# Kernel optimization log

Hardware: AMD Instinct MI355X
Metric: run time of the kernel (lower is better)

Reference implementation:

```python
import jax, jax.numpy as jnp
import numpy as np

D_MODEL = 768
NUM_HEADS = 12
HEAD_DIM = D_MODEL // NUM_HEADS
ROPE_THETA = 10000.0
MAX_SEQ_LEN = 2048
BATCH = 2
SEQ = 2048


def _rope_tables():
    # powers = arange(0, d_k, 2)/d_k ; freqs = theta**-powers ; angles = t outer freqs
    powers = jnp.arange(0, HEAD_DIM, 2, dtype=jnp.float32) / HEAD_DIM
    freqs = 1.0 / (ROPE_THETA ** powers)                      # [d_k/2]
    t = jnp.arange(MAX_SEQ_LEN, dtype=jnp.float32)
    angles = t[:, None] * freqs[None, :]                      # [max_seq_len, d_k/2]
    return jnp.cos(angles), jnp.sin(angles)


def _apply_rope(x, cos, sin, pos):
    # x: [b, h, s, d], pos: [b, s]; interleaved even/odd pairing
    c = cos[pos][:, None]          # [b, 1, s, d/2]
    s = sin[pos][:, None]
    x_even = x[..., 0::2]
    x_odd = x[..., 1::2]
    new_even = x_even * c - x_odd * s
    new_odd = x_even * s + x_odd * c
    # re-interleave: (..., f, 2) -> (..., 2f)
    return jnp.stack([new_even, new_odd], axis=-1).reshape(x.shape)


def setup_inputs() -> dict:
    key = jax.random.key(0)
    k1, k2, k3 = jax.random.split(key, 3)
    x = jax.random.normal(k1, (BATCH, SEQ, D_MODEL), dtype=jnp.float32)
    token_positions = jnp.broadcast_to(jnp.arange(SEQ, dtype=jnp.int32), (BATCH, SEQ))
    sigma_qkv = (2.0 / (D_MODEL + 3 * D_MODEL)) ** 0.5
    sigma_o = (2.0 / (D_MODEL + D_MODEL)) ** 0.5
    W_qkv = jax.random.normal(k2, (3 * D_MODEL, D_MODEL), dtype=jnp.float32) * sigma_qkv
    W_o = jax.random.normal(k3, (D_MODEL, D_MODEL), dtype=jnp.float32) * sigma_o
    return {"x": x, "token_positions": token_positions, "W_qkv": W_qkv, "W_o": W_o}


def reference(x, token_positions, W_qkv, W_o):
    b, s, _ = x.shape
    cos, sin = _rope_tables()
    qkv = jnp.einsum('bsd,ed->bse', x, W_qkv)                 # [b, s, 3*d_model]
    qkv = qkv.reshape(b, s, 3, NUM_HEADS, HEAD_DIM)
    qkv = jnp.transpose(qkv, (2, 0, 3, 1, 4))                 # [3, b, h, s, hd]
    q, k, v = qkv[0], qkv[1], qkv[2]
    q = _apply_rope(q, cos, sin, token_positions)
    k = _apply_rope(k, cos, sin, token_positions)
    scores = jnp.einsum('bhqd,bhkd->bhqk', q, k) / (HEAD_DIM ** 0.5)
    causal = jnp.tril(jnp.ones((s, s), dtype=bool))
    scores = jnp.where(causal, scores, -jnp.inf)
    weights = jax.nn.softmax(scores, axis=-1)
    context = jnp.einsum('bhqk,bhkd->bhqd', weights, v)
    context = jnp.transpose(context, (0, 2, 1, 3)).reshape(b, s, D_MODEL)
    return jnp.einsum('bsd,ed->bse', context, W_o)
```

## Files before the change

### kernel.cpp

```cpp
#include <hip/hip_runtime.h>
#include <hip/hip_bf16.h>
#include <math.h>

#define SEQ 2048
#define DM 768
#define NH 12
#define HD 64
#define NB 2
#define NT (NB*SEQ)
#define E3 (3*DM)

using short4v = __attribute__((ext_vector_type(4))) short;
using short8v = __attribute__((ext_vector_type(8))) short;
using floatx4 = __attribute__((ext_vector_type(4))) float;
using int4v   = __attribute__((ext_vector_type(4))) int;

#if __has_builtin(__builtin_amdgcn_exp2f)
#define EXPFN(x) __builtin_amdgcn_exp2f(x)
#define QSCALE 0.1803368801111244f
#else
#define EXPFN(x) __expf(x)
#define QSCALE 0.125f
#endif

static __device__ __forceinline__ short bfb(float f) {
  union { __hip_bfloat16 h; short s; } u;
  u.h = __float2bfloat16(f);
  return u.s;
}

static __device__ __forceinline__ void gload_lds16(const __hip_bfloat16* g, __hip_bfloat16* lds) {
  __builtin_amdgcn_global_load_lds(
      (const __attribute__((address_space(1))) unsigned int*)g,
      (__attribute__((address_space(3))) unsigned int*)lds, 16, 0, 0);
}

static __device__ __forceinline__ int swzg(int row) {
  return (((row >> 3) & 3) + 2 * (row & 3)) & 7;
}

#define XN4 (NT * DM / 4)
#define WQN4 (E3 * DM / 4)
#define WON4 (DM * DM / 4)
#define CVT_N (XN4 + WQN4 + WON4)
__global__ void cvt3_rope(const float* __restrict__ x, const float* __restrict__ wq,
                          const float* __restrict__ wo,
                          __hip_bfloat16* __restrict__ xb, __hip_bfloat16* __restrict__ wqb,
                          __hip_bfloat16* __restrict__ wob, float2* __restrict__ rcs,
                          int* __restrict__ qcnt) {
  int i = blockIdx.x * blockDim.x + threadIdx.x;
  if (blockIdx.x == 0 && threadIdx.x < 8) qcnt[threadIdx.x] = 0;
  if (i >= CVT_N) {
    int idx = i - CVT_N;
    if (idx < SEQ * 32) {
      int pos = idx >> 5, j = idx & 31;
      float freq = __expf(-(float)j * (logf(10000.0f) / 32.0f));
      float ang = (float)pos * freq;
      rcs[idx] = make_float2(cosf(ang), sinf(ang));
    }
    return;
  }
  const float* src;
  __hip_bfloat16* dst;
  int k;
  if (i < XN4) { src = x; dst = xb; k = i; }
  else if (i < XN4 + WQN4) { src = wq; dst = wqb; k = i - XN4; }
  else { src = wo; dst = wob; k = i - XN4 - WQN4; }
  floatx4 v = ((const floatx4*)src)[k];
  short4v o;
  o[0] = bfb(v[0]); o[1] = bfb(v[1]); o[2] = bfb(v[2]); o[3] = bfb(v[3]);
  ((short4v*)dst)[k] = o;
}

__global__ __launch_bounds__(256) void qkv_gemm_rope(
    const __hip_bfloat16* __restrict__ Wq,
    const __hip_bfloat16* __restrict__ Xb,
    const int* __restrict__ tpos,
    const float2* __restrict__ rcs,
    __hip_bfloat16* __restrict__ Qb, __hip_bfloat16* __restrict__ Kb,
    __hip_bfloat16* __restrict__ Vt)
{
  __shared__ __align__(16) __hip_bfloat16 As[2][64 * 64];
  __shared__ __align__(16) __hip_bfloat16 Bs[2][128 * 64];
  const int tid = threadIdx.x;
  const int lane = tid & 63, w = tid >> 6;
  const int c = lane & 15, g = lane >> 4;
  const int wr = w >> 1, wc = w & 1;
  const int bid = blockIdx.x;
  const int xcd = bid & 7, i_ = bid >> 3;
  const int nb = xcd * 4 + (i_ & 3), mb = i_ >> 2;
  const int m0 = mb * 64, n0 = nb * 128;
  const int srow = tid >> 3, sslot = tid & 7;

#define QKV_STAGE(K0_, AD, BD)                                                      \
  do {                                                                              \
    _Pragma("unroll")                                                               \
    for (int j = 0; j < 2; ++j) {                                                   \
      const int row = j * 32 + srow;                                                \
      const int gs = (sslot ^ (row & 7)) * 8;                                       \
      gload_lds16(Wq + (size_t)(m0 + row) * DM + (K0_) + gs, (AD) + j * 2048 + w * 512); \
    }                                                                               \
    _Pragma("unroll")                                                               \
    for (int j = 0; j < 4; ++j) {                                                   \
      const int row = j * 32 + srow;                                                \
      const int gs = (sslot ^ (row & 7)) * 8;                                       \
      gload_lds16(Xb + (size_t)(n0 + row) * DM + (K0_) + gs, (BD) + j * 2048 + w * 512); \
    }                                                                               \
  } while (0)

  floatx4 acc[2][4] = {};
  QKV_STAGE(0, As[0], Bs[0]);
  int cb = 0;
  for (int k0 = 0; k0 < DM; k0 += 64) {
    if (k0 + 64 < DM) QKV_STAGE(k0 + 64, As[cb ^ 1], Bs[cb ^ 1]);
    __syncthreads();
#pragma unroll
    for (int kk = 0; kk < 2; ++kk) {
      short8v a[2], b[4];
#pragma unroll
      for (int i = 0; i < 2; ++i) {
        const int row = wr * 32 + i * 16 + c;
        a[i] = *(const short8v*)&As[cb][row * 64 + (((kk * 4 + g) ^ (row & 7)) * 8)];
      }
#pragma unroll
      for (int j = 0; j < 4; ++j) {
        const int row = wc * 64 + j * 16 + c;
        b[j] = *(const short8v*)&Bs[cb][row * 64 + (((kk * 4 + g) ^ (row & 7)) * 8)];
      }
#pragma unroll
      for (int i = 0; i < 2; ++i)
#pragma unroll
        for (int j = 0; j < 4; ++j)
          acc[i][j] = __builtin_amdgcn_mfma_f32_16x16x32_bf16(a[i], b[j], acc[i][j], 0, 0, 0);
    }
    __syncthreads();
    cb ^= 1;
  }
#undef QKV_STAGE
#pragma unroll
  for (int i = 0; i < 2; ++i) {
    const int e0 = m0 + wr * 32 + i * 16 + 4 * g;
    const int jj = (e0 & 63) >> 1;
#pragma unroll
    for (int j = 0; j < 4; ++j) {
      const int t = n0 + wc * 64 + j * 16 + c;
      const int b_ = t >> 11, s = t & (SEQ - 1);
      float v0 = acc[i][j][0], v1 = acc[i][j][1], v2 = acc[i][j][2], v3 = acc[i][j][3];
      if (e0 < 2 * DM) {
        const int pos = tpos[t];
        const float2 cs0 = rcs[pos * 32 + jj];
        const float2 cs1 = rcs[pos * 32 + jj + 1];
        const float n0v = v0 * cs0.x - v1 * cs0.y, n1v = v0 * cs0.y + v1 * cs0.x;
        const float n2v = v2 * cs1.x - v3 * cs1.y, n3v = v2 * cs1.y + v3 * cs1.x;
        v0 = n0v; v1 = n1v; v2 = n2v; v3 = n3v;
      }
      if (e0 < DM) {
        const int h = e0 >> 6, d = e0 & 63;
        short4v pk;
        pk[0] = bfb(v0 * QSCALE); pk[1] = bfb(v1 * QSCALE);
        pk[2] = bfb(v2 * QSCALE); pk[3] = bfb(v3 * QSCALE);
        *(short4v*)&Qb[(((size_t)(b_ * NH + h) * SEQ) + s) * HD + d] = pk;
      } else if (e0 < 2 * DM) {
        const int e = e0 - DM, h = e >> 6, d = e & 63;
        short4v pk;
        pk[0] = bfb(v0); pk[1] = bfb(v1); pk[2] = bfb(v2); pk[3] = bfb(v3);
        *(short4v*)&Kb[(((size_t)(b_ * NH + h) * SEQ) + s) * HD + d] = pk;
      } else {
        const int e = e0 - 2 * DM, h = e >> 6, d = e & 63;
        const size_t base = ((size_t)(b_ * NH + h) * HD + d) * SEQ + s;
        Vt[base]           = __float2bfloat16(v0);
        Vt[base + SEQ]     = __float2bfloat16(v1);
        Vt[base + 2 * SEQ] = __float2bfloat16(v2);
        Vt[base + 3 * SEQ] = __float2bfloat16(v3);
      }
    }
  }
}

__global__ __launch_bounds__(512) void attn_fused(
    const __hip_bfloat16* __restrict__ Qb,
    const __hip_bfloat16* __restrict__ Kb,
    const __hip_bfloat16* __restrict__ Vt,
    __hip_bfloat16* __restrict__ Cx,
    int* __restrict__ qcnt)
{
  __shared__ __align__(16) __hip_bfloat16 Ks[2][128 * 64];
  __shared__ __align__(16) __hip_bfloat16 Vs[2][64 * 128];
  __shared__ int task_s;
  const int tid = threadIdx.x;
  const int lane = tid & 63, w = tid >> 6;
  const int c = lane & 15, g = lane >> 4;
  const int xcd = blockIdx.x & 7;
  const int kr1 = 8 * (c >> 2) + (c & 3);
  const int ksr = w * 8 + (lane >> 3), kss = lane & 7;
  const int vsr = w * 4 + (lane >> 4), vss = lane & 15;

  for (;;) {
    if (tid == 0) task_s = atomicAdd(&qcnt[xcd], 1);
    __syncthreads();
    const int task = task_s;
    if (task >= 48) return;
    const int qG = 15 - task / 3;
    const int bh = xcd + 8 * (task % 3);
    const int KBmax = qG;
    const __hip_bfloat16* Qh = Qb + (size_t)bh * SEQ * HD;
    const __hip_bfloat16* Kh = Kb + (size_t)bh * SEQ * HD;
    const __hip_bfloat16* Vh = Vt + (size_t)bh * HD * SEQ;
    const int q1 = qG * 128 + w * 16 + c;
    const int qrl32 = (w & 1) * 16 + c;
    const int sdiag = w >> 1;
    const short8v qf10 = *(const short8v*)&Qh[(size_t)q1 * HD + g * 8];
    const short8v qf11 = *(const short8v*)&Qh[(size_t)q1 * HD + 32 + g * 8];
    floatx4 o1[4] = {};
    float l1 = 0.0f;

#define STAGE_KV(KB_, KSD, VSD)                                                      \
    do {                                                                             \
      _Pragma("unroll")                                                              \
      for (int j = 0; j < 2; ++j) {                                                  \
        const int kr = j * 64 + ksr;                                                 \
        gload_lds16(Kh + (size_t)((KB_) * 128 + kr) * HD + ((kss ^ swzg(kr)) * 8),   \
                    (KSD) + j * 4096 + w * 512);                                     \
        const int vr = j * 32 + vsr;                                                 \
        gload_lds16(Vh + (size_t)vr * SEQ + (KB_) * 128 + ((vss ^ (vr & 15)) * 8),   \
                    (VSD) + j * 4096 + w * 512);                                     \
      }                                                                              \
    } while (0)

#define SUBBLK(S_, DO_MASK)                                                          \
    do {                                                                             \
      const int r0 = (S_) * 32 + kr1, r1 = r0 + 4;                                   \
      const int z0 = swzg(r0), z1 = swzg(r1);                                        \
      const short8v a00 = *(const short8v*)&Kt[r0 * 64 + ((g ^ z0) * 8)];            \
      const short8v a01 = *(const short8v*)&Kt[r0 * 64 + (((4 + g) ^ z0) * 8)];      \
      const short8v a10 = *(const short8v*)&Kt[r1 * 64 + ((g ^ z1) * 8)];            \
      const short8v a11 = *(const short8v*)&Kt[r1 * 64 + (((4 + g) ^ z1) * 8)];      \
      short8v vf[4];                                                                 \
      _Pragma("unroll")                                                              \
      for (int f = 0; f < 4; ++f) {                                                  \
        const int rv = f * 16 + c;                                                   \
        vf[f] = *(const short8v*)&Vb[rv * 128 + ((((S_) * 4 + g) ^ (rv & 15)) * 8)]; \
      }                                                                              \
      floatx4 s1a = {}, s1b = {};                                                    \
      __builtin_amdgcn_s_setprio(1);                                                 \
      s1a = __builtin_amdgcn_mfma_f32_16x16x32_bf16(a00, qf10, s1a, 0, 0, 0);        \
      s1a = __builtin_amdgcn_mfma_f32_16x16x32_bf16(a01, qf11, s1a, 0, 0, 0);        \
      s1b = __builtin_amdgcn_mfma_f32_16x16x32_bf16(a10, qf10, s1b, 0, 0, 0);        \
      s1b = __builtin_amdgcn_mfma_f32_16x16x32_bf16(a11, qf11, s1b, 0, 0, 0);        \
      __builtin_amdgcn_s_setprio(0);                                                 \
      if (DO_MASK) {                                                                 \
        _Pragma("unroll")                                                            \
        for (int r = 0; r < 4; ++r) {                                                \
          if (8 * g + r > qrl32) s1a[r] = -INFINITY;                                 \
          if (8 * g + r + 4 > qrl32) s1b[r] = -INFINITY;                             \
        }                                                                            \
      }                                                                              \
      short8v pf1;                                                                   \
      _Pragma("unroll")                                                              \
      for (int r = 0; r < 4; ++r) {                                                  \
        float p;                                                                     \
        p = EXPFN(s1a[r]); l1 += p; pf1[r] = bfb(p);                                 \
        p = EXPFN(s1b[r]); l1 += p; pf1[r + 4] = bfb(p);                             \
      }                                                                              \
      __builtin_amdgcn_s_setprio(1);                                                 \
      o1[0] = __builtin_amdgcn_mfma_f32_16x16x32_bf16(vf[0], pf1, o1[0], 0, 0, 0);   \
      o1[1] = __builtin_amdgcn_mfma_f32_16x16x32_bf16(vf[1], pf1, o1[1], 0, 0, 0);   \
      o1[2] = __builtin_amdgcn_mfma_f32_16x16x32_bf16(vf[2], pf1, o1[2], 0, 0, 0);   \
      o1[3] = __builtin_amdgcn_mfma_f32_16x16x32_bf16(vf[3], pf1, o1[3], 0, 0, 0);   \
      __builtin_amdgcn_s_setprio(0);                                                 \
    } while (0)

    STAGE_KV(0, Ks[0], Vs[0]);
    __syncthreads();
    int cb = 0;
    for (int kb = 0; kb <= KBmax; ++kb) {
      if (kb < KBmax) STAGE_KV(kb + 1, Ks[cb ^ 1], Vs[cb ^ 1]);
      {
        const __hip_bfloat16* Kt = Ks[cb];
        const __hip_bfloat16* Vb = Vs[cb];
        if (kb < KBmax) {
          SUBBLK(0, false);
          SUBBLK(1, false);
          SUBBLK(2, false);
          SUBBLK(3, false);
        } else {
#pragma unroll
          for (int s = 0; s < 4; ++s) {
            if (s < sdiag) SUBBLK(s, false);
            else if (s == sdiag) SUBBLK(s, true);
          }
        }
      }
      __syncthreads();
      cb ^= 1;
    }
#undef SUBBLK
#undef STAGE_KV

    l1 += __shfl_xor(l1, 16); l1 += __shfl_xor(l1, 32);
    const float inv1 = 1.0f / l1;
    const int bb = bh / NH, h = bh - bb * NH;
    const size_t trow1 = ((size_t)bb * SEQ + q1) * DM + (size_t)h * HD;
#pragma unroll
    for (int f = 0; f < 4; ++f) {
      short4v pk1;
#pragma unroll
      for (int r = 0; r < 4; ++r) pk1[r] = bfb(o1[f][r] * inv1);
      *(short4v*)&Cx[trow1 + f * 16 + 4 * g] = pk1;
    }
  }
}

__global__ __launch_bounds__(256) void out_gemm(
    const __hip_bfloat16* __restrict__ Wo,
    const __hip_bfloat16* __restrict__ Cx,
    float* __restrict__ out)
{
  __shared__ __align__(16) __hip_bfloat16 As[2][64 * 64];
  __shared__ __align__(16) __hip_bfloat16 Bs[2][128 * 64];
  const int tid = threadIdx.x;
  const int lane = tid & 63, w = tid >> 6;
  const int c = lane & 15, g = lane >> 4;
  const int wr = w >> 1, wc = w & 1;
  const int bid = blockIdx.x;
  const int xcd = bid & 7, i_ = bid >> 3;
  const int nb = xcd * 4 + (i_ & 3), mb = i_ >> 2;
  const int m0 = mb * 64, n0 = nb * 128;
  const int srow = tid >> 3, sslot = tid & 7;

#define OUT_STAGE(K0_, AD, BD)                                                      \
  do {                                                                              \
    _Pragma("unroll")                                                               \
    for (int j = 0; j < 2; ++j) {                                                   \
      const int row = j * 32 + srow;                                                \
      const int gs = (sslot ^ (row & 7)) * 8;                                       \
      gload_lds16(Wo + (size_t)(m0 + row) * DM + (K0_) + gs, (AD) + j * 2048 + w * 512); \
    }                                                                               \
    _Pragma("unroll")                                                               \
    for (int j = 0; j < 4; ++j) {                                                   \
      const int row = j * 32 + srow;                                                \
      const int gs = (sslot ^ (row & 7)) * 8;                                       \
      gload_lds16(Cx + (size_t)(n0 + row) * DM + (K0_) + gs, (BD) + j * 2048 + w * 512); \
    }                                                                               \
  } while (0)

  floatx4 acc[2][4] = {};
  OUT_STAGE(0, As[0], Bs[0]);
  int cb = 0;
  for (int k0 = 0; k0 < DM; k0 += 64) {
    if (k0 + 64 < DM) OUT_STAGE(k0 + 64, As[cb ^ 1], Bs[cb ^ 1]);
    __syncthreads();
#pragma unroll
    for (int kk = 0; kk < 2; ++kk) {
      short8v a[2], b[4];
#pragma unroll
      for (int i = 0; i < 2; ++i) {
        const int row = wr * 32 + i * 16 + c;
        a[i] = *(const short8v*)&As[cb][row * 64 + (((kk * 4 + g) ^ (row & 7)) * 8)];
      }
#pragma unroll
      for (int j = 0; j < 4; ++j) {
        const int row = wc * 64 + j * 16 + c;
        b[j] = *(const short8v*)&Bs[cb][row * 64 + (((kk * 4 + g) ^ (row & 7)) * 8)];
      }
#pragma unroll
      for (int i = 0; i < 2; ++i)
#pragma unroll
        for (int j = 0; j < 4; ++j)
          acc[i][j] = __builtin_amdgcn_mfma_f32_16x16x32_bf16(a[i], b[j], acc[i][j], 0, 0, 0);
    }
    __syncthreads();
    cb ^= 1;
  }
#undef OUT_STAGE
#pragma unroll
  for (int i = 0; i < 2; ++i) {
    const int e0 = m0 + wr * 32 + i * 16 + 4 * g;
#pragma unroll
    for (int j = 0; j < 4; ++j) {
      const int t = n0 + wc * 64 + j * 16 + c;
      *(floatx4*)&out[(size_t)t * DM + e0] = acc[i][j];
    }
  }
}

extern "C" void kernel_launch(void* const* d_in, const int* in_sizes, int n_in,
                              void* d_out, int out_size, void* d_ws, size_t ws_size,
                              hipStream_t stream) {
  const float* x    = (const float*)d_in[0];
  const int*   tpos = (const int*)d_in[1];
  const float* Wq   = (const float*)d_in[2];
  const float* Wo   = (const float*)d_in[3];
  float* out = (float*)d_out;

  const size_t QKV_BYTES = (size_t)NB * NH * SEQ * HD * 2;
  const size_t REQUIRED = 4 * QKV_BYTES;
  if (ws_size < REQUIRED) return;

  char* ws = (char*)d_ws;
  __hip_bfloat16* Qb = (__hip_bfloat16*)(ws);
  __hip_bfloat16* Kb = (__hip_bfloat16*)(ws + QKV_BYTES);
  __hip_bfloat16* Vt = (__hip_bfloat16*)(ws + 2 * QKV_BYTES);
  __hip_bfloat16* Cx = (__hip_bfloat16*)(ws + 3 * QKV_BYTES);
  __hip_bfloat16* xb = (__hip_bfloat16*)(ws + 3 * QKV_BYTES);
  char* ob = (char*)d_out;
  float2* rcs = (float2*)(ob);
  __hip_bfloat16* wqb = (__hip_bfloat16*)(ob + (size_t)SEQ * 32 * 8);
  __hip_bfloat16* wob = (__hip_bfloat16*)(ob + (size_t)SEQ * 32 * 8 + (size_t)E3 * DM * 2);
  int* qcnt = (int*)(ob + (size_t)SEQ * 32 * 8 + (size_t)E3 * DM * 2 + (size_t)DM * DM * 2);

  const int TOT_N = CVT_N + SEQ * 32;
  cvt3_rope<<<dim3((TOT_N + 255) / 256), dim3(256), 0, stream>>>(x, Wq, Wo, xb, wqb, wob, rcs, qcnt);
  qkv_gemm_rope<<<dim3(1152), dim3(256), 0, stream>>>(wqb, xb, tpos, rcs, Qb, Kb, Vt);
  attn_fused<<<dim3(512), dim3(512), 0, stream>>>(Qb, Kb, Vt, Cx, qcnt);
  out_gemm<<<dim3(384), dim3(256), 0, stream>>>(wob, Cx, out);
}
```

Baseline: 83.35 us.

## Halve attention block to 4 waves, each computing two 16-row query tiles

```diff
diff --git a/kernel.cpp b/kernel.cpp
--- a/kernel.cpp
+++ b/kernel.cpp
@@ -177,7 +177,7 @@
   }
 }
 
-__global__ __launch_bounds__(512) void attn_fused(
+__global__ __launch_bounds__(256) void attn_fused(
     const __hip_bfloat16* __restrict__ Qb,
     const __hip_bfloat16* __restrict__ Kb,
     const __hip_bfloat16* __restrict__ Vt,
@@ -192,8 +192,6 @@
   const int c = lane & 15, g = lane >> 4;
   const int xcd = blockIdx.x & 7;
   const int kr1 = 8 * (c >> 2) + (c & 3);
-  const int ksr = w * 8 + (lane >> 3), kss = lane & 7;
-  const int vsr = w * 4 + (lane >> 4), vss = lane & 15;
 
   for (;;) {
     if (tid == 0) task_s = atomicAdd(&qcnt[xcd], 1);
@@ -206,24 +204,26 @@
     const __hip_bfloat16* Qh = Qb + (size_t)bh * SEQ * HD;
     const __hip_bfloat16* Kh = Kb + (size_t)bh * SEQ * HD;
     const __hip_bfloat16* Vh = Vt + (size_t)bh * HD * SEQ;
-    const int q1 = qG * 128 + w * 16 + c;
-    const int qrl32 = (w & 1) * 16 + c;
-    const int sdiag = w >> 1;
-    const short8v qf10 = *(const short8v*)&Qh[(size_t)q1 * HD + g * 8];
-    const short8v qf11 = *(const short8v*)&Qh[(size_t)q1 * HD + 32 + g * 8];
-    floatx4 o1[4] = {};
-    float l1 = 0.0f;
+    const int q1 = qG * 128 + w * 32 + c;
+    const int q2 = q1 + 16;
+    const short8v qfA0 = *(const short8v*)&Qh[(size_t)q1 * HD + g * 8];
+    const short8v qfA1 = *(const short8v*)&Qh[(size_t)q1 * HD + 32 + g * 8];
+    const short8v qfB0 = *(const short8v*)&Qh[(size_t)q2 * HD + g * 8];
+    const short8v qfB1 = *(const short8v*)&Qh[(size_t)q2 * HD + 32 + g * 8];
+    floatx4 o1[4] = {}, o2[4] = {};
+    float l1 = 0.0f, l2 = 0.0f;
 
 #define STAGE_KV(KB_, KSD, VSD)                                                      \
     do {                                                                             \
       _Pragma("unroll")                                                              \
-      for (int j = 0; j < 2; ++j) {                                                  \
-        const int kr = j * 64 + ksr;                                                 \
-        gload_lds16(Kh + (size_t)((KB_) * 128 + kr) * HD + ((kss ^ swzg(kr)) * 8),   \
-                    (KSD) + j * 4096 + w * 512);                                     \
-        const int vr = j * 32 + vsr;                                                 \
-        gload_lds16(Vh + (size_t)vr * SEQ + (KB_) * 128 + ((vss ^ (vr & 15)) * 8),   \
-                    (VSD) + j * 4096 + w * 512);                                     \
+      for (int j = 0; j < 4; ++j) {                                                  \
+        const int i4 = 4 * w + j;                                                    \
+        const int kr = i4 * 8 + (lane >> 3);                                         \
+        gload_lds16(Kh + (size_t)((KB_) * 128 + kr) * HD + (((lane & 7) ^ swzg(kr)) * 8), \
+                    (KSD) + i4 * 512);                                               \
+        const int vr = i4 * 4 + (lane >> 4);                                         \
+        gload_lds16(Vh + (size_t)vr * SEQ + (KB_) * 128 + (((lane & 15) ^ (vr & 15)) * 8), \
+                    (VSD) + i4 * 512);                                               \
       }                                                                              \
     } while (0)
 
@@ -241,32 +241,45 @@
         const int rv = f * 16 + c;                                                   \
         vf[f] = *(const short8v*)&Vb[rv * 128 + ((((S_) * 4 + g) ^ (rv & 15)) * 8)]; \
       }                                                                              \
-      floatx4 s1a = {}, s1b = {};                                                    \
+      floatx4 s1a = {}, s1b = {}, s2a = {}, s2b = {};                                \
       __builtin_amdgcn_s_setprio(1);                                                 \
-      s1a = __builtin_amdgcn_mfma_f32_16x16x32_bf16(a00, qf10, s1a, 0, 0, 0);        \
-      s1a = __builtin_amdgcn_mfma_f32_16x16x32_bf16(a01, qf11, s1a, 0, 0, 0);        \
-      s1b = __builtin_amdgcn_mfma_f32_16x16x32_bf16(a10, qf10, s1b, 0, 0, 0);        \
-      s1b = __builtin_amdgcn_mfma_f32_16x16x32_bf16(a11, qf11, s1b, 0, 0, 0);        \
+      s1a = __builtin_amdgcn_mfma_f32_16x16x32_bf16(a00, qfA0, s1a, 0, 0, 0);        \
+      s1a = __builtin_amdgcn_mfma_f32_16x16x32_bf16(a01, qfA1, s1a, 0, 0, 0);        \
+      s1b = __builtin_amdgcn_mfma_f32_16x16x32_bf16(a10, qfA0, s1b, 0, 0, 0);        \
+      s1b = __builtin_amdgcn_mfma_f32_16x16x32_bf16(a11, qfA1, s1b, 0, 0, 0);        \
+      s2a = __builtin_amdgcn_mfma_f32_16x16x32_bf16(a00, qfB0, s2a, 0, 0, 0);        \
+      s2a = __builtin_amdgcn_mfma_f32_16x16x32_bf16(a01, qfB1, s2a, 0, 0, 0);        \
+      s2b = __builtin_amdgcn_mfma_f32_16x16x32_bf16(a10, qfB0, s2b, 0, 0, 0);        \
+      s2b = __builtin_amdgcn_mfma_f32_16x16x32_bf16(a11, qfB1, s2b, 0, 0, 0);        \
       __builtin_amdgcn_s_setprio(0);                                                 \
       if (DO_MASK) {                                                                 \
         _Pragma("unroll")                                                            \
         for (int r = 0; r < 4; ++r) {                                                \
-          if (8 * g + r > qrl32) s1a[r] = -INFINITY;                                 \
-          if (8 * g + r + 4 > qrl32) s1b[r] = -INFINITY;                             \
+          const int kt = 8 * g + r;                                                  \
+          if (kt > c) s1a[r] = -INFINITY;                                            \
+          if (kt + 4 > c) s1b[r] = -INFINITY;                                        \
+          if (kt > 16 + c) s2a[r] = -INFINITY;                                       \
+          if (kt + 4 > 16 + c) s2b[r] = -INFINITY;                                   \
         }                                                                            \
       }                                                                              \
-      short8v pf1;                                                                   \
+      short8v pf1, pf2;                                                              \
       _Pragma("unroll")                                                              \
       for (int r = 0; r < 4; ++r) {                                                  \
         float p;                                                                     \
         p = EXPFN(s1a[r]); l1 += p; pf1[r] = bfb(p);                                 \
         p = EXPFN(s1b[r]); l1 += p; pf1[r + 4] = bfb(p);                             \
+        p = EXPFN(s2a[r]); l2 += p; pf2[r] = bfb(p);                                 \
+        p = EXPFN(s2b[r]); l2 += p; pf2[r + 4] = bfb(p);                             \
       }                                                                              \
       __builtin_amdgcn_s_setprio(1);                                                 \
       o1[0] = __builtin_amdgcn_mfma_f32_16x16x32_bf16(vf[0], pf1, o1[0], 0, 0, 0);   \
       o1[1] = __builtin_amdgcn_mfma_f32_16x16x32_bf16(vf[1], pf1, o1[1], 0, 0, 0);   \
       o1[2] = __builtin_amdgcn_mfma_f32_16x16x32_bf16(vf[2], pf1, o1[2], 0, 0, 0);   \
       o1[3] = __builtin_amdgcn_mfma_f32_16x16x32_bf16(vf[3], pf1, o1[3], 0, 0, 0);   \
+      o2[0] = __builtin_amdgcn_mfma_f32_16x16x32_bf16(vf[0], pf2, o2[0], 0, 0, 0);   \
+      o2[1] = __builtin_amdgcn_mfma_f32_16x16x32_bf16(vf[1], pf2, o2[1], 0, 0, 0);   \
+      o2[2] = __builtin_amdgcn_mfma_f32_16x16x32_bf16(vf[2], pf2, o2[2], 0, 0, 0);   \
+      o2[3] = __builtin_amdgcn_mfma_f32_16x16x32_bf16(vf[3], pf2, o2[3], 0, 0, 0);   \
       __builtin_amdgcn_s_setprio(0);                                                 \
     } while (0)
 
@@ -286,8 +299,8 @@
         } else {
 #pragma unroll
           for (int s = 0; s < 4; ++s) {
-            if (s < sdiag) SUBBLK(s, false);
-            else if (s == sdiag) SUBBLK(s, true);
+            if (s < w) SUBBLK(s, false);
+            else if (s == w) SUBBLK(s, true);
           }
         }
       }
@@ -298,15 +311,21 @@
 #undef STAGE_KV
 
     l1 += __shfl_xor(l1, 16); l1 += __shfl_xor(l1, 32);
-    const float inv1 = 1.0f / l1;
+    l2 += __shfl_xor(l2, 16); l2 += __shfl_xor(l2, 32);
+    const float inv1 = 1.0f / l1, inv2 = 1.0f / l2;
     const int bb = bh / NH, h = bh - bb * NH;
     const size_t trow1 = ((size_t)bb * SEQ + q1) * DM + (size_t)h * HD;
+    const size_t trow2 = trow1 + (size_t)16 * DM;
 #pragma unroll
     for (int f = 0; f < 4; ++f) {
-      short4v pk1;
-#pragma unroll
-      for (int r = 0; r < 4; ++r) pk1[r] = bfb(o1[f][r] * inv1);
+      short4v pk1, pk2;
+#pragma unroll
+      for (int r = 0; r < 4; ++r) {
+        pk1[r] = bfb(o1[f][r] * inv1);
+        pk2[r] = bfb(o2[f][r] * inv2);
+      }
       *(short4v*)&Cx[trow1 + f * 16 + 4 * g] = pk1;
+      *(short4v*)&Cx[trow2 + f * 16 + 4 * g] = pk2;
     }
   }
 }
@@ -412,6 +431,6 @@
   const int TOT_N = CVT_N + SEQ * 32;
   cvt3_rope<<<dim3((TOT_N + 255) / 256), dim3(256), 0, stream>>>(x, Wq, Wo, xb, wqb, wob, rcs, qcnt);
   qkv_gemm_rope<<<dim3(1152), dim3(256), 0, stream>>>(wqb, xb, tpos, rcs, Qb, Kb, Vt);
-  attn_fused<<<dim3(512), dim3(512), 0, stream>>>(Qb, Kb, Vt, Cx, qcnt);
+  attn_fused<<<dim3(512), dim3(256), 0, stream>>>(Qb, Kb, Vt, Cx, qcnt);
   out_gemm<<<dim3(384), dim3(256), 0, stream>>>(wob, Cx, out);
 }
```

Measured after the change: 88.12 us. 1.06x slower.
